# Kernel optimization log

Measured on AMD Instinct MI355X. Metric: run time of the kernel, lower is better.

Reference implementation:

```python
import jax, jax.numpy as jnp
import numpy as np

N_NODES = 16384
N_EDGES = 131072
N_GRAPHS = 16
U_SZ, U_RED = 4096, 256
EDGE_H, EDGE_OUT = 1024, 512
NODE_H = 512
NODE_IN = 9  # 4 + 5, hard-coded in OGRENet
EDGE_IN = 1


def _lin_init(k, fan_in, fan_out):
    k1, k2 = jax.random.split(k)
    bound = 1.0 / np.sqrt(fan_in)
    W = jax.random.uniform(k1, (fan_in, fan_out), jnp.float32, -bound, bound)
    b = jax.random.uniform(k2, (fan_out,), jnp.float32, -bound, bound)
    return W, b


def setup_inputs() -> dict:
    key = jax.random.key(0)
    ks = jax.random.split(key, 16)
    inp = {
        "x": jax.random.normal(ks[0], (N_NODES, NODE_IN), jnp.float32),
        "edge_attr": jax.random.normal(ks[1], (N_EDGES, EDGE_IN), jnp.float32),
        "u": jax.random.normal(ks[2], (N_GRAPHS, U_SZ), jnp.float32),
        "edge_index": jax.random.randint(ks[3], (2, N_EDGES), 0, N_NODES, jnp.int64 if jax.config.jax_enable_x64 else jnp.int32).astype(jnp.int32),
        "batch": jnp.sort(jax.random.randint(ks[4], (N_NODES,), 0, N_GRAPHS)).astype(jnp.int32),
    }
    # global dim reduction 4096 -> 256
    inp["w_dr"], inp["b_dr"] = _lin_init(ks[5], U_SZ, U_RED)
    # edge MLP: in = 1 + 2*9 + 256 = 275
    e_in = EDGE_IN + 2 * NODE_IN + U_RED
    inp["e_w0"], inp["e_b0"] = _lin_init(ks[6], e_in, EDGE_H)
    inp["e_w1"], inp["e_b1"] = _lin_init(ks[7], EDGE_H, EDGE_H)
    inp["e_w2"], inp["e_b2"] = _lin_init(ks[8], EDGE_H, EDGE_H)
    inp["e_w3"], inp["e_b3"] = _lin_init(ks[9], EDGE_H, EDGE_H)
    inp["e_wf"], inp["e_bf"] = _lin_init(ks[10], EDGE_H, EDGE_OUT)
    # node mlp 1: in = 9 + 512 = 521
    inp["n1_w0"], inp["n1_b0"] = _lin_init(ks[11], NODE_IN + EDGE_OUT, NODE_H)
    inp["n1_w1"], inp["n1_b1"] = _lin_init(ks[12], NODE_H, NODE_H)
    # node mlp 2: in = 9 + 512 + 256 = 777, out = 1
    inp["n2_w0"], inp["n2_b0"] = _lin_init(ks[13], NODE_IN + NODE_H + U_RED, NODE_H)
    inp["n2_w1"], inp["n2_b1"] = _lin_init(ks[14], NODE_H, 1)
    return inp


def reference(x, edge_attr, u, edge_index, batch,
              w_dr, b_dr,
              e_w0, e_b0, e_w1, e_b1, e_w2, e_b2, e_w3, e_b3, e_wf, e_bf,
              n1_w0, n1_b0, n1_w1, n1_b1,
              n2_w0, n2_b0, n2_w1, n2_b1):
    relu = jax.nn.relu
    # select_dim_reduction
    u_r = u @ w_dr + b_dr  # [G, 256]
    row, col = edge_index[0], edge_index[1]
    # EdgeModel: cat([src, dest, edge_attr, u[batch[row]]])
    e_in = jnp.concatenate([x[row], x[col], edge_attr, u_r[batch[row]]], axis=1)
    h = relu(e_in @ e_w0 + e_b0)
    h = relu(h @ e_w1 + e_b1)
    h = relu(h @ e_w2 + e_b2)
    h = relu(h @ e_w3 + e_b3)
    e = h @ e_wf + e_bf  # [E, 512]
    # NodeModel: mlp1 on cat([x[col], edge_attr_new]) then scatter_mean by row
    n_in = jnp.concatenate([x[col], e], axis=1)
    h = relu(n_in @ n1_w0 + n1_b0)
    h = relu(h @ n1_w1 + n1_b1)  # [E, 512]
    agg = jax.ops.segment_sum(h, row, num_segments=N_NODES)
    cnt = jax.ops.segment_sum(jnp.ones((h.shape[0],), h.dtype), row, num_segments=N_NODES)
    agg = agg / jnp.maximum(cnt, 1.0)[:, None]  # scatter_mean (zeros stay zero)
    o = jnp.concatenate([x, agg, u_r[batch]], axis=1)
    o = relu(o @ n2_w0 + n2_b0) @ n2_w1 + n2_b1  # [N, 1]
    return jnp.squeeze(o, axis=-1)
```

## Files before the change

### kernel.cpp

```cpp
#include <hip/hip_runtime.h>
#include <type_traits>
#include <utility>
#include <cstdint>

typedef unsigned short u16;
typedef __attribute__((ext_vector_type(4))) float f32x4;
typedef __attribute__((ext_vector_type(8))) short s16x8;
typedef __attribute__((ext_vector_type(8))) __bf16 b16x8;

template <typename T, typename = void> struct MfmaTakes : std::false_type {};
template <typename T>
struct MfmaTakes<T, std::void_t<decltype(__builtin_amdgcn_mfma_f32_16x16x32_bf16(
    std::declval<T>(), std::declval<T>(), std::declval<f32x4>(), 0, 0, 0))>>
    : std::true_type {};
using abvec = std::conditional_t<MfmaTakes<s16x8>::value, s16x8, b16x8>;
static_assert(sizeof(abvec) == 16, "frag must be 4 VGPRs");

template <typename T>
__device__ __forceinline__ f32x4 mfma_bf16(T a, T b, f32x4 c) {
  return __builtin_amdgcn_mfma_f32_16x16x32_bf16(a, b, c, 0, 0, 0);
}

__device__ __forceinline__ float b2f(u16 v) {
  union { unsigned u; float f; } x; x.u = ((unsigned)v) << 16; return x.f;
}
__device__ __forceinline__ u16 f2b(float f) {
  union { float f; unsigned u; } x; x.f = f;
  unsigned r = x.u + 0x7fffu + ((x.u >> 16) & 1u);
  return (u16)(r >> 16);
}

__device__ __forceinline__ void gld16(const void* g, void* l) {
  auto gp = reinterpret_cast<const __attribute__((address_space(1))) unsigned int*>(
      reinterpret_cast<uintptr_t>(g));
  auto lp = reinterpret_cast<__attribute__((address_space(3))) unsigned int*>(
      reinterpret_cast<uintptr_t>(l));
  __builtin_amdgcn_global_load_lds(gp, lp, 16, 0, 0);
}

#define NN 16384
#define NE 131072
#define NG 16

__global__ void detect_dtype(const u16* __restrict__ x, int* __restrict__ flag) {
  __shared__ int cnt;
  if (threadIdx.x == 0) cnt = 0;
  __syncthreads();
  int local = 0;
#pragma unroll
  for (int i = 0; i < 8; i++) {
    u16 h = x[threadIdx.x * 8 + i];
    int e = (h >> 7) & 0xFF;
    if (h == 0 || (e >= 110 && e <= 134)) local++;
  }
  atomicAdd(&cnt, local);
  __syncthreads();
  if (threadIdx.x == 0) *flag = (cnt >= 1700) ? 1 : 0;
}

struct CvtJob {
  const void* src[14];
  void* dst[14];
  int n[14];
};

__global__ __launch_bounds__(256) void cvt_all(CvtJob jb, const int* __restrict__ flag) {
  const int idx = blockIdx.x * 256 + threadIdx.x;
  const int f = *flag;
  int off = 0;
#pragma unroll
  for (int j = 0; j < 14; j++) {
    const int nn = jb.n[j];
    if (idx < off + nn) {
      const int i = idx - off;
      u16 v = f ? ((const u16*)jb.src[j])[i]
                : f2b(((const float*)jb.src[j])[i]);
      ((u16*)jb.dst[j])[i] = v;
      return;
    }
    off += nn;
  }
}

__global__ __launch_bounds__(256) void cvt_plain(
    const void* __restrict__ src, u16* __restrict__ dst, int n,
    const int* __restrict__ flag)
{
  const int i = blockIdx.x * 256 + threadIdx.x;
  if (i >= n) return;
  dst[i] = *flag ? ((const u16*)src)[i] : f2b(((const float*)src)[i]);
}

__global__ __launch_bounds__(256, 3) void gemm_bt(
    const u16* __restrict__ A, const u16* __restrict__ Bt,
    const u16* __restrict__ bias, u16* __restrict__ C,
    int M, int N, int K, int ldc, int relu)
{
  __shared__ alignas(16) u16 smem[24576];
  const int tid = threadIdx.x;
  const int wave = tid >> 6, lane = tid & 63;
  const int m0 = blockIdx.x * 128, n0 = blockIdx.y * 128;

  const int srow = lane >> 2;
  const int kslot = lane & 3;
  const int sswz = (srow >> 1) & 3;
  const u16* gA = A + (size_t)(m0 + wave * 32 + srow) * K + (kslot ^ sswz) * 8;
  const u16* gB = Bt + (size_t)(n0 + wave * 32 + srow) * K + (kslot ^ sswz) * 8;
  const int loff = (wave * 32 + srow) * 32 + kslot * 8;

  const int wm = (wave >> 1) * 64;
  const int wn = (wave & 1) * 64;
  const int fr = lane & 15;
  const int fks = ((lane >> 4) ^ ((fr >> 1) & 3)) * 8;

  f32x4 acc[4][4] = {};
  const int NT = K >> 5;

#define STAGE(t, s) do { \
    const int o_ = (t) * 32; \
    u16* S_ = smem + (s) * 8192; \
    gld16(gA + o_, S_ + loff); gld16(gA + 16 * (size_t)K + o_, S_ + loff + 512); \
    gld16(gB + o_, S_ + 4096 + loff); gld16(gB + 16 * (size_t)K + o_, S_ + 4096 + loff + 512); \
  } while (0)

  STAGE(0, 0);
  if (NT > 1) {
    STAGE(1, 1);
    __asm__ volatile("s_waitcnt vmcnt(4)" ::: "memory");
  } else {
    __asm__ volatile("s_waitcnt vmcnt(0)" ::: "memory");
  }
  __builtin_amdgcn_s_barrier();

  int sl = 0;
  for (int t = 0; t < NT; t++) {
    if (t + 2 < NT) {
      const int sw = (sl + 2 >= 3) ? sl - 1 : sl + 2;
      STAGE(t + 2, sw);
    }
    const u16* As = smem + sl * 8192;
    const u16* Bs = As + 4096;
    abvec af[4], bf[4];
#pragma unroll
    for (int i = 0; i < 4; i++)
      af[i] = *(const abvec*)&As[(wm + i * 16 + fr) * 32 + fks];
#pragma unroll
    for (int i = 0; i < 4; i++)
      bf[i] = *(const abvec*)&Bs[(wn + i * 16 + fr) * 32 + fks];
    __builtin_amdgcn_s_setprio(1);
#pragma unroll
    for (int mi = 0; mi < 4; mi++)
#pragma unroll
      for (int ni = 0; ni < 4; ni++)
        acc[mi][ni] = mfma_bf16(af[mi], bf[ni], acc[mi][ni]);
    __builtin_amdgcn_s_setprio(0);
    if (t + 2 < NT) __asm__ volatile("s_waitcnt vmcnt(4)" ::: "memory");
    else            __asm__ volatile("s_waitcnt vmcnt(0)" ::: "memory");
    __builtin_amdgcn_s_barrier();
    sl = (sl == 2) ? 0 : sl + 1;
  }
#undef STAGE

  const int crow0 = (lane >> 4) * 4;
  float bv[4];
#pragma unroll
  for (int ni = 0; ni < 4; ni++) bv[ni] = b2f(bias[n0 + wn + ni * 16 + fr]);

  u16* W = smem + wave * 4096;
#pragma unroll
  for (int mi = 0; mi < 4; mi++) {
#pragma unroll
    for (int ni = 0; ni < 4; ni++) {
      f32x4 v = acc[mi][ni];
      const int colx = ni * 16 + fr;
      const int cl = colx & 7, ch = colx >> 3;
#pragma unroll
      for (int r = 0; r < 4; r++) {
        const int rowx = mi * 16 + crow0 + r;
        float f = v[r] + bv[ni];
        if (relu) f = fmaxf(f, 0.0f);
        W[rowx * 64 + ((ch ^ (rowx & 7)) << 3) + cl] = f2b(f);
      }
    }
  }
  __asm__ volatile("s_waitcnt lgkmcnt(0)" ::: "memory");
#pragma unroll
  for (int p = 0; p < 8; p++) {
    const int rowx = p * 8 + (lane >> 3);
    const int pc = lane & 7;
    const int lc = pc ^ (rowx & 7);
    s16x8 val = *(const s16x8*)&W[rowx * 64 + pc * 8];
    *(s16x8*)&C[(size_t)(m0 + wm + rowx) * ldc + n0 + wn + lc * 8] = val;
  }
}

__global__ __launch_bounds__(256, 3) void gemm_bt_rb(
    const u16* __restrict__ A, const u16* __restrict__ Bt,
    const u16* __restrict__ bias, u16* __restrict__ C,
    int M, int N, int K, int ldc, int relu,
    const u16* __restrict__ rb, const int* __restrict__ ridx, int rbs)
{
  __shared__ alignas(16) u16 smem[24576];
  const int tid = threadIdx.x;
  const int wave = tid >> 6, lane = tid & 63;
  const int m0 = blockIdx.x * 128, n0 = blockIdx.y * 128;

  const int srow = lane >> 2;
  const int kslot = lane & 3;
  const int sswz = (srow >> 1) & 3;
  const u16* gA = A + (size_t)(m0 + wave * 32 + srow) * K + (kslot ^ sswz) * 8;
  const u16* gB = Bt + (size_t)(n0 + wave * 32 + srow) * K + (kslot ^ sswz) * 8;
  const int loff = (wave * 32 + srow) * 32 + kslot * 8;

  const int wm = (wave >> 1) * 64;
  const int wn = (wave & 1) * 64;
  const int fr = lane & 15;
  const int fks = ((lane >> 4) ^ ((fr >> 1) & 3)) * 8;

  f32x4 acc[4][4] = {};
  const int NT = K >> 5;

#define STAGE(t, s) do { \
    const int o_ = (t) * 32; \
    u16* S_ = smem + (s) * 8192; \
    gld16(gA + o_, S_ + loff); gld16(gA + 16 * (size_t)K + o_, S_ + loff + 512); \
    gld16(gB + o_, S_ + 4096 + loff); gld16(gB + 16 * (size_t)K + o_, S_ + 4096 + loff + 512); \
  } while (0)

  STAGE(0, 0);
  if (NT > 1) {
    STAGE(1, 1);
    __asm__ volatile("s_waitcnt vmcnt(4)" ::: "memory");
  } else {
    __asm__ volatile("s_waitcnt vmcnt(0)" ::: "memory");
  }
  __builtin_amdgcn_s_barrier();

  int sl = 0;
  for (int t = 0; t < NT; t++) {
    if (t + 2 < NT) {
      const int sw = (sl + 2 >= 3) ? sl - 1 : sl + 2;
      STAGE(t + 2, sw);
    }
    const u16* As = smem + sl * 8192;
    const u16* Bs = As + 4096;
    abvec af[4], bf[4];
#pragma unroll
    for (int i = 0; i < 4; i++)
      af[i] = *(const abvec*)&As[(wm + i * 16 + fr) * 32 + fks];
#pragma unroll
    for (int i = 0; i < 4; i++)
      bf[i] = *(const abvec*)&Bs[(wn + i * 16 + fr) * 32 + fks];
    __builtin_amdgcn_s_setprio(1);
#pragma unroll
    for (int mi = 0; mi < 4; mi++)
#pragma unroll
      for (int ni = 0; ni < 4; ni++)
        acc[mi][ni] = mfma_bf16(af[mi], bf[ni], acc[mi][ni]);
    __builtin_amdgcn_s_setprio(0);
    if (t + 2 < NT) __asm__ volatile("s_waitcnt vmcnt(4)" ::: "memory");
    else            __asm__ volatile("s_waitcnt vmcnt(0)" ::: "memory");
    __builtin_amdgcn_s_barrier();
    sl = (sl == 2) ? 0 : sl + 1;
  }
#undef STAGE

  const int crow0 = (lane >> 4) * 4;
  float bv[4];
#pragma unroll
  for (int ni = 0; ni < 4; ni++) bv[ni] = b2f(bias[n0 + wn + ni * 16 + fr]);

  u16* W = smem + wave * 4096;
#pragma unroll
  for (int mi = 0; mi < 4; mi++) {
#pragma unroll
    for (int ni = 0; ni < 4; ni++) {
      f32x4 v = acc[mi][ni];
      const int colx = ni * 16 + fr;
      const int cl = colx & 7, ch = colx >> 3;
#pragma unroll
      for (int r = 0; r < 4; r++) {
        const int rowx = mi * 16 + crow0 + r;
        float f = v[r] + bv[ni]
                + b2f(rb[(size_t)ridx[m0 + wm + rowx] * rbs + n0 + wn + ni * 16 + fr]);
        if (relu) f = fmaxf(f, 0.0f);
        W[rowx * 64 + ((ch ^ (rowx & 7)) << 3) + cl] = f2b(f);
      }
    }
  }
  __asm__ volatile("s_waitcnt lgkmcnt(0)" ::: "memory");
#pragma unroll
  for (int p = 0; p < 8; p++) {
    const int rowx = p * 8 + (lane >> 3);
    const int pc = lane & 7;
    const int lc = pc ^ (rowx & 7);
    s16x8 val = *(const s16x8*)&W[rowx * 64 + pc * 8];
    *(s16x8*)&C[(size_t)(m0 + wm + rowx) * ldc + n0 + wn + lc * 8] = val;
  }
}

__global__ __launch_bounds__(1024) void gemm256b(
    const u16* __restrict__ A, const u16* __restrict__ Bt,
    const u16* __restrict__ bias, u16* __restrict__ C,
    int K, int ldc, int relu)
{
  __shared__ alignas(16) u16 smem[49152];
  const int tid = threadIdx.x;
  const int wave = tid >> 6, lane = tid & 63;
  const int wr = wave >> 2, wc = wave & 3;
  const int m0 = blockIdx.x << 8, n0 = blockIdx.y << 8;

  const int srow = tid >> 2;
  const int kslot = tid & 3;
  const int sswz = (srow >> 1) & 3;
  const u16* gA = A  + (size_t)(m0 + srow) * K + (kslot ^ sswz) * 8;
  const u16* gB = Bt + (size_t)(n0 + srow) * K + (kslot ^ sswz) * 8;
  const int loff = tid * 8;

  const int fr = lane & 15;
  const int fks = ((lane >> 4) ^ ((fr >> 1) & 3)) * 8;
  const int aob = (wr * 64 + fr) * 32 + fks;
  const int bob = (wc * 64 + fr) * 32 + fks;

  f32x4 acc[4][4] = {};
  const int NT = K >> 5;

#define STAGE2(t, s) do { \
    const int o_ = (t) * 32; \
    u16* S_ = smem + (s) * 16384; \
    gld16(gA + o_, S_ + loff); gld16(gB + o_, S_ + 8192 + loff); \
  } while (0)

  STAGE2(0, 0);
  if (NT > 1) {
    STAGE2(1, 1);
    __asm__ volatile("s_waitcnt vmcnt(2)" ::: "memory");
  } else {
    __asm__ volatile("s_waitcnt vmcnt(0)" ::: "memory");
  }
  __builtin_amdgcn_s_barrier();

  int sl = 0;
  for (int t = 0; t < NT; t++) {
    if (t + 2 < NT) {
      const int sw = (sl + 2 >= 3) ? sl - 1 : sl + 2;
      STAGE2(t + 2, sw);
    }
    const u16* As = smem + sl * 16384;
    const u16* Bs = As + 8192;
    abvec af[4], bf[4];
#pragma unroll
    for (int i = 0; i < 4; i++)
      af[i] = *(const abvec*)&As[aob + i * 512];
#pragma unroll
    for (int i = 0; i < 4; i++)
      bf[i] = *(const abvec*)&Bs[bob + i * 512];
    __builtin_amdgcn_s_setprio(1);
#pragma unroll
    for (int mi = 0; mi < 4; mi++)
#pragma unroll
      for (int ni = 0; ni < 4; ni++)
        acc[mi][ni] = mfma_bf16(af[mi], bf[ni], acc[mi][ni]);
    __builtin_amdgcn_s_setprio(0);
    if (t + 2 < NT) __asm__ volatile("s_waitcnt vmcnt(2)" ::: "memory");
    else            __asm__ volatile("s_waitcnt vmcnt(0)" ::: "memory");
    __builtin_amdgcn_s_barrier();
    sl = (sl == 2) ? 0 : sl + 1;
  }
#undef STAGE2

  const int crow0 = (lane >> 4) * 4;
  float bv[4];
#pragma unroll
  for (int ni = 0; ni < 4; ni++) bv[ni] = b2f(bias[n0 + wc * 64 + ni * 16 + fr]);
  u16* W = smem + wave * 2048;
#pragma unroll
  for (int h = 0; h < 2; h++) {
    if (h) __asm__ volatile("s_waitcnt lgkmcnt(0)" ::: "memory");
#pragma unroll
    for (int mi = 0; mi < 4; mi++) {
#pragma unroll
      for (int nh = 0; nh < 2; nh++) {
        const int ni = h * 2 + nh;
        f32x4 v = acc[mi][ni];
        const int colx = nh * 16 + fr;
        const int cl = colx & 7, ch = colx >> 3;
#pragma unroll
        for (int r = 0; r < 4; r++) {
          const int rowx = mi * 16 + crow0 + r;
          float f = v[r] + bv[ni];
          if (relu) f = fmaxf(f, 0.0f);
          W[rowx * 32 + ((ch ^ (rowx & 3)) << 3) + cl] = f2b(f);
        }
      }
    }
    __asm__ volatile("s_waitcnt lgkmcnt(0)" ::: "memory");
#pragma unroll
    for (int p = 0; p < 4; p++) {
      const int rowx = p * 16 + (lane >> 2);
      const int pc = lane & 3;
      const int lc = pc ^ (rowx & 3);
      s16x8 val = *(const s16x8*)&W[rowx * 32 + pc * 8];
      *(s16x8*)&C[(size_t)(m0 + wr * 64 + rowx) * ldc + n0 + wc * 64 + h * 32 + lc * 8] = val;
    }
  }
}

__global__ __launch_bounds__(1024) void gemm256b_rb(
    const u16* __restrict__ A, const u16* __restrict__ Bt,
    const u16* __restrict__ bias, u16* __restrict__ C,
    int K, int ldc, int relu,
    const u16* __restrict__ rb, const int* __restrict__ ridx, int rbs)
{
  __shared__ alignas(16) u16 smem[49152];
  const int tid = threadIdx.x;
  const int wave = tid >> 6, lane = tid & 63;
  const int wr = wave >> 2, wc = wave & 3;
  const int m0 = blockIdx.x << 8, n0 = blockIdx.y << 8;

  const int srow = tid >> 2;
  const int kslot = tid & 3;
  const int sswz = (srow >> 1) & 3;
  const u16* gA = A  + (size_t)(m0 + srow) * K + (kslot ^ sswz) * 8;
  const u16* gB = Bt + (size_t)(n0 + srow) * K + (kslot ^ sswz) * 8;
  const int loff = tid * 8;

  const int fr = lane & 15;
  const int fks = ((lane >> 4) ^ ((fr >> 1) & 3)) * 8;
  const int aob = (wr * 64 + fr) * 32 + fks;
  const int bob = (wc * 64 + fr) * 32 + fks;

  f32x4 acc[4][4] = {};
  const int NT = K >> 5;

#define STAGE2(t, s) do { \
    const int o_ = (t) * 32; \
    u16* S_ = smem + (s) * 16384; \
    gld16(gA + o_, S_ + loff); gld16(gB + o_, S_ + 8192 + loff); \
  } while (0)

  STAGE2(0, 0);
  if (NT > 1) {
    STAGE2(1, 1);
    __asm__ volatile("s_waitcnt vmcnt(2)" ::: "memory");
  } else {
    __asm__ volatile("s_waitcnt vmcnt(0)" ::: "memory");
  }
  __builtin_amdgcn_s_barrier();

  int sl = 0;
  for (int t = 0; t < NT; t++) {
    if (t + 2 < NT) {
      const int sw = (sl + 2 >= 3) ? sl - 1 : sl + 2;
      STAGE2(t + 2, sw);
    }
    const u16* As = smem + sl * 16384;
    const u16* Bs = As + 8192;
    abvec af[4], bf[4];
#pragma unroll
    for (int i = 0; i < 4; i++)
      af[i] = *(const abvec*)&As[aob + i * 512];
#pragma unroll
    for (int i = 0; i < 4; i++)
      bf[i] = *(const abvec*)&Bs[bob + i * 512];
    __builtin_amdgcn_s_setprio(1);
#pragma unroll
    for (int mi = 0; mi < 4; mi++)
#pragma unroll
      for (int ni = 0; ni < 4; ni++)
        acc[mi][ni] = mfma_bf16(af[mi], bf[ni], acc[mi][ni]);
    __builtin_amdgcn_s_setprio(0);
    if (t + 2 < NT) __asm__ volatile("s_waitcnt vmcnt(2)" ::: "memory");
    else            __asm__ volatile("s_waitcnt vmcnt(0)" ::: "memory");
    __builtin_amdgcn_s_barrier();
    sl = (sl == 2) ? 0 : sl + 1;
  }
#undef STAGE2

  const int crow0 = (lane >> 4) * 4;
  float bv[4];
#pragma unroll
  for (int ni = 0; ni < 4; ni++) bv[ni] = b2f(bias[n0 + wc * 64 + ni * 16 + fr]);
  u16* W = smem + wave * 2048;
#pragma unroll
  for (int h = 0; h < 2; h++) {
    if (h) __asm__ volatile("s_waitcnt lgkmcnt(0)" ::: "memory");
#pragma unroll
    for (int mi = 0; mi < 4; mi++) {
#pragma unroll
      for (int nh = 0; nh < 2; nh++) {
        const int ni = h * 2 + nh;
        f32x4 v = acc[mi][ni];
        const int colx = nh * 16 + fr;
        const int cl = colx & 7, ch = colx >> 3;
#pragma unroll
        for (int r = 0; r < 4; r++) {
          const int rowx = mi * 16 + crow0 + r;
          float f = v[r] + bv[ni]
                  + b2f(rb[(size_t)ridx[m0 + wr * 64 + rowx] * rbs + n0 + wc * 64 + ni * 16 + fr]);
          if (relu) f = fmaxf(f, 0.0f);
          W[rowx * 32 + ((ch ^ (rowx & 3)) << 3) + cl] = f2b(f);
        }
      }
    }
    __asm__ volatile("s_waitcnt lgkmcnt(0)" ::: "memory");
#pragma unroll
    for (int p = 0; p < 4; p++) {
      const int rowx = p * 16 + (lane >> 2);
      const int pc = lane & 3;
      const int lc = pc ^ (rowx & 3);
      s16x8 val = *(const s16x8*)&W[rowx * 32 + pc * 8];
      *(s16x8*)&C[(size_t)(m0 + wr * 64 + rowx) * ldc + n0 + wc * 64 + h * 32 + lc * 8] = val;
    }
  }
}

__global__ __launch_bounds__(256) void transpose_pad(
    const void* __restrict__ src, u16* __restrict__ dst, int K, int N, int Kp,
    int perm, int k0, const int* __restrict__ flag)
{
  __shared__ u16 tile[32][33];
  const int f = *flag;
  const u16* s16p = (const u16*)src;
  const float* sfp = (const float*)src;
  const int kb = blockIdx.x * 32, nb = blockIdx.y * 32;
  const int tx = threadIdx.x & 31, ty = threadIdx.x >> 5;
#pragma unroll
  for (int i = 0; i < 32; i += 8) {
    int k = kb + ty + i, n = nb + tx;
    u16 v = 0;
    if (k < K && n < N)
      v = f ? s16p[(size_t)(k0 + k) * N + n] : f2b(sfp[(size_t)(k0 + k) * N + n]);
    tile[ty + i][tx] = v;
  }
  __syncthreads();
#pragma unroll
  for (int i = 0; i < 32; i += 8) {
    int n = nb + ty + i, k = kb + tx;
    if (n < N && k < Kp) {
      int nk = perm ? (k < 9 ? 512 + k : (k < 521 ? k - 9 : k)) : k;
      dst[(size_t)n * Kp + nk] = tile[tx][ty + i];
    }
  }
}

__global__ __launch_bounds__(256) void fuse_tail(
    const u16* __restrict__ n1w0t, u16* __restrict__ fused)
{
  const int idx = blockIdx.x * 256 + threadIdx.x;
  const int p = idx >> 5, t = idx & 31;
  fused[p * 1056 + 1024 + t] = n1w0t[p * 544 + 512 + t];
}

__global__ __launch_bounds__(256) void fuse_bias(
    const u16* __restrict__ ebf, const u16* __restrict__ n1b0,
    const u16* __restrict__ n1w0e, u16* __restrict__ fb)
{
  const int p = blockIdx.x * 256 + threadIdx.x;
  float acc = b2f(n1b0[p]);
#pragma unroll 8
  for (int j = 0; j < 512; j++) acc += b2f(ebf[j]) * b2f(n1w0e[p * 512 + j]);
  fb[p] = f2b(acc);
}

__global__ __launch_bounds__(256) void make_uwb(
    const void* __restrict__ w0, const u16* __restrict__ ur,
    const u16* __restrict__ eb0, u16* __restrict__ uwb,
    const int* __restrict__ flag)
{
  const int g = blockIdx.x;
  const int n = blockIdx.y * 256 + threadIdx.x;
  const int f = *flag;
  __shared__ u16 us[256];
  us[threadIdx.x] = ur[g * 256 + threadIdx.x];
  __syncthreads();
  float acc = b2f(eb0[n]);
  if (f) {
    const u16* wp = (const u16*)w0 + 19ull * 1024 + n;
#pragma unroll 8
    for (int j = 0; j < 256; j++) acc += b2f(us[j]) * b2f(wp[(size_t)j * 1024]);
  } else {
    const float* wp = (const float*)w0 + 19ull * 1024 + n;
#pragma unroll 8
    for (int j = 0; j < 256; j++) acc += b2f(us[j]) * wp[(size_t)j * 1024];
  }
  uwb[g * 1024 + n] = f2b(acc);
}

__global__ __launch_bounds__(256) void make_uw2(
    const void* __restrict__ w, const u16* __restrict__ ur,
    const u16* __restrict__ b0, u16* __restrict__ uw2,
    const int* __restrict__ flag)
{
  const int g = blockIdx.x;
  const int p = blockIdx.y * 256 + threadIdx.x;
  const int f = *flag;
  __shared__ u16 us[256];
  us[threadIdx.x] = ur[g * 256 + threadIdx.x];
  __syncthreads();
  float acc = b2f(b0[p]);
  if (f) {
    const u16* wp = (const u16*)w + 521ull * 512 + p;
#pragma unroll 8
    for (int j = 0; j < 256; j++) acc += b2f(us[j]) * b2f(wp[(size_t)j * 512]);
  } else {
    const float* wp = (const float*)w + 521ull * 512 + p;
#pragma unroll 8
    for (int j = 0; j < 256; j++) acc += b2f(us[j]) * wp[(size_t)j * 512];
  }
  uw2[g * 512 + p] = f2b(acc);
}

__global__ __launch_bounds__(256) void dim_reduce2(
    const u16* __restrict__ u, const void* __restrict__ w,
    float* __restrict__ uacc, const int* __restrict__ flag)
{
  const int g = blockIdx.x, kt = blockIdx.y, j = threadIdx.x;
  const int f = *flag;
  __shared__ u16 us[512];
  us[j] = u[g * 4096 + kt * 512 + j];
  us[256 + j] = u[g * 4096 + kt * 512 + 256 + j];
  __syncthreads();
  float acc = 0.0f;
  if (f) {
    const u16* wp = (const u16*)w + (size_t)(kt * 512) * 256 + j;
#pragma unroll 8
    for (int k = 0; k < 512; k++) acc += b2f(us[k]) * b2f(wp[(size_t)k * 256]);
  } else {
    const float* wp = (const float*)w + (size_t)(kt * 512) * 256 + j;
#pragma unroll 8
    for (int k = 0; k < 512; k++) acc += b2f(us[k]) * wp[(size_t)k * 256];
  }
  atomicAdd(&uacc[g * 256 + j], acc);
}

__global__ __launch_bounds__(256) void finish_ur(
    const float* __restrict__ uacc, const u16* __restrict__ bdr,
    u16* __restrict__ ur)
{
  const int i = blockIdx.x * 256 + threadIdx.x;
  ur[i] = f2b(uacc[i] + b2f(bdr[i & 255]));
}

__global__ __launch_bounds__(256) void count_edges(
    const int* __restrict__ row, int* __restrict__ cnt)
{
  const int e = blockIdx.x * 256 + threadIdx.x;
  if (e < NE) atomicAdd(&cnt[row[e]], 1);
}

__global__ __launch_bounds__(256) void prefix_offs(
    const int* __restrict__ cnt, int* __restrict__ offs, int* __restrict__ cursor)
{
  __shared__ int part[256];
  __shared__ int base[256];
  const int t = threadIdx.x;
  int s = 0;
#pragma unroll
  for (int i = 0; i < 64; i++) s += cnt[t * 64 + i];
  part[t] = s;
  __syncthreads();
  if (t == 0) {
    int r = 0;
    for (int i = 0; i < 256; i++) { base[i] = r; r += part[i]; }
  }
  __syncthreads();
  int r = base[t];
#pragma unroll
  for (int i = 0; i < 64; i++) {
    const int n = t * 64 + i;
    offs[n] = r; cursor[n] = r; r += cnt[n];
  }
  if (t == 255) offs[16384] = r;
}

__global__ __launch_bounds__(256) void build_perm(
    const int* __restrict__ row, int* __restrict__ cursor, int* __restrict__ eperm)
{
  const int e = blockIdx.x * 256 + threadIdx.x;
  const int pos = atomicAdd(&cursor[row[e]], 1);
  eperm[pos] = e;
}

__global__ __launch_bounds__(256) void build_ein2(
    const u16* __restrict__ x, const u16* __restrict__ ea,
    const int* __restrict__ row, const int* __restrict__ col,
    const int* __restrict__ batch, const int* __restrict__ eperm,
    u16* __restrict__ out, int* __restrict__ bidx, int e0)
{
  const int idx = blockIdx.x * 256 + threadIdx.x;
  const int le = idx >> 2, g = idx & 3;
  const int c0 = g * 8;
  const int e = eperm[e0 + le];
  const int r = row[e];
  const int cl = col[e];
  if (g == 0) bidx[le] = batch[r];
  alignas(16) u16 v[8];
#pragma unroll
  for (int j = 0; j < 8; j++) {
    const int c = c0 + j;
    u16 t;
    if (c < 9)        t = x[r * 9 + c];
    else if (c < 18)  t = x[cl * 9 + (c - 9)];
    else if (c == 18) t = ea[e];
    else              t = 0;
    v[j] = t;
  }
  *(s16x8*)&out[(size_t)le * 32 + c0] = *(const s16x8*)v;
}

__global__ __launch_bounds__(256) void fill_h_tail(
    const u16* __restrict__ x, const int* __restrict__ col,
    const int* __restrict__ eperm, u16* __restrict__ out, int e0)
{
  const int idx = blockIdx.x * 256 + threadIdx.x;
  const int le = idx >> 2, j8 = idx & 3;
  const int c0 = 1024 + j8 * 8;
  const int cl = col[eperm[e0 + le]];
  alignas(16) u16 v[8];
#pragma unroll
  for (int j = 0; j < 8; j++) {
    const int c = c0 + j;
    v[j] = (c < 1033) ? x[cl * 9 + (c - 1024)] : (u16)0;
  }
  *(s16x8*)&out[(size_t)le * 1056 + c0] = *(const s16x8*)v;
}

__global__ __launch_bounds__(256) void seg_reduce(
    const u16* __restrict__ h, const int* __restrict__ offs,
    float* __restrict__ agg, int e0, int echunk)
{
  const int wave = threadIdx.x >> 6, lane = threadIdx.x & 63;
  const int n = blockIdx.x * 4 + wave;
  int lo = offs[n], hi = offs[n + 1];
  const int first = (lo >= e0);
  lo = lo > e0 ? lo : e0;
  const int e1 = e0 + echunk;
  hi = hi < e1 ? hi : e1;
  if (lo >= hi) return;
  const int c0 = lane * 8;
  float acc[8] = {};
  for (int i = lo; i < hi; i++) {
    s16x8 v = *(const s16x8*)&h[(size_t)(i - e0) * 512 + c0];
#pragma unroll
    for (int j = 0; j < 8; j++) acc[j] += b2f((u16)v[j]);
  }
  float* ap = &agg[(size_t)n * 512 + c0];
  if (first) {
#pragma unroll
    for (int j = 0; j < 8; j++) ap[j] = acc[j];
  } else {
#pragma unroll
    for (int j = 0; j < 8; j++) ap[j] += acc[j];
  }
}

__global__ __launch_bounds__(256) void build_nin2(
    const u16* __restrict__ x, const float* __restrict__ agg,
    const int* __restrict__ cnt, u16* __restrict__ out, int n0)
{
  const int idx = blockIdx.x * 256 + threadIdx.x;
  const int le = idx / 68, g = idx % 68;
  const int c0 = g * 8;
  const int n = n0 + le;
  alignas(16) u16 v[8];
  if (c0 < 512) {
    const int cn = cnt[n];
    if (cn == 0) {
#pragma unroll
      for (int j = 0; j < 8; j++) v[j] = 0;
    } else {
      const float den = (float)cn;
      const f32x4* ap = (const f32x4*)&agg[(size_t)n * 512 + c0];
      f32x4 a0 = ap[0], a1 = ap[1];
#pragma unroll
      for (int j = 0; j < 4; j++) { v[j] = f2b(a0[j] / den); v[4 + j] = f2b(a1[j] / den); }
    }
  } else {
#pragma unroll
    for (int j = 0; j < 8; j++) {
      const int c = c0 + j;
      v[j] = (c < 521) ? x[n * 9 + (c - 512)] : (u16)0;
    }
  }
  *(s16x8*)&out[(size_t)le * 544 + c0] = *(const s16x8*)v;
}

__global__ __launch_bounds__(256) void final_dot(
    const u16* __restrict__ h, const u16* __restrict__ w,
    const u16* __restrict__ b, void* __restrict__ out, int n0,
    const int* __restrict__ flag)
{
  const int wave = threadIdx.x >> 6, lane = threadIdx.x & 63;
  const int n = blockIdx.x * 4 + wave;
  const u16* hp = h + (size_t)n * 512 + lane * 8;
  const u16* wp = w + lane * 8;
  float s = 0.0f;
#pragma unroll
  for (int i = 0; i < 8; i++) s += b2f(hp[i]) * b2f(wp[i]);
#pragma unroll
  for (int off = 32; off > 0; off >>= 1) s += __shfl_down(s, off, 64);
  if (lane == 0) {
    float r = s + b2f(b[0]);
    if (*flag) ((u16*)out)[n0 + n] = f2b(r);
    else       ((float*)out)[n0 + n] = r;
  }
}

constexpr size_t OFF_FLAG = 0;
constexpr size_t OFF_XC   = 64;
constexpr size_t OFF_EAC  = OFF_XC   + 147456ull * 2;
constexpr size_t OFF_UC   = OFF_EAC  + 131072ull * 2;
constexpr size_t OFF_BDR  = OFF_UC   + 65536ull * 2;
constexpr size_t OFF_EB0  = OFF_BDR  + 256ull * 2;
constexpr size_t OFF_EB1  = OFF_EB0  + 1024ull * 2;
constexpr size_t OFF_EB2  = OFF_EB1  + 1024ull * 2;
constexpr size_t OFF_EB3  = OFF_EB2  + 1024ull * 2;
constexpr size_t OFF_EBF  = OFF_EB3  + 1024ull * 2;
constexpr size_t OFF_N1B0 = OFF_EBF  + 512ull * 2;
constexpr size_t OFF_N1B1 = OFF_N1B0 + 512ull * 2;
constexpr size_t OFF_N2B0 = OFF_N1B1 + 512ull * 2;
constexpr size_t OFF_N2W1 = OFF_N2B0 + 512ull * 2;
constexpr size_t OFF_N2B1 = OFF_N2W1 + 512ull * 2;
constexpr size_t OFF_OFFS = (OFF_N2B1 + 64 + 63) & ~63ull;
constexpr size_t OFF_CUR  = OFF_OFFS + 16388ull * 4;
constexpr size_t OFF_UACC = OFF_CUR  + 16384ull * 4;
static_assert(OFF_UACC + 4096 * 4 < (1ull << 20), "params+small fit in 1MB");

constexpr size_t OFF_W0T  = 1ull << 20;
constexpr size_t OFF_W1T  = OFF_W0T  + 1024ull * 320 * 2;
constexpr size_t OFF_W2T  = OFF_W1T  + 1024ull * 1024 * 2;
constexpr size_t OFF_W3T  = OFF_W2T  + 1024ull * 1024 * 2;
constexpr size_t OFF_WFC  = OFF_W3T  + 1024ull * 1024 * 2;
constexpr size_t OFF_N1W0 = OFF_WFC  + 1024ull * 512 * 2;
constexpr size_t OFF_N1W1 = OFF_N1W0 + 512ull * 544 * 2;
constexpr size_t OFF_N2W0 = OFF_N1W1 + 512ull * 512 * 2;
constexpr size_t OFF_N1WE = OFF_N2W0 + 512ull * 800 * 2;
constexpr size_t OFF_FUSE = OFF_N1WE + 512ull * 512 * 2;
constexpr size_t OFF_FB   = OFF_FUSE + 512ull * 1056 * 2;
constexpr size_t OFF_ZB   = OFF_FB   + 512ull * 2;
constexpr size_t OFF_UWB  = OFF_ZB   + 1024ull * 2;
constexpr size_t OFF_UW2  = OFF_UWB  + 16384ull * 2;
constexpr size_t OFF_UR   = OFF_UW2  + 8192ull * 2;
constexpr size_t OFF_CNT  = OFF_UR   + 16ull * 256 * 2;
constexpr size_t OFF_AGG  = OFF_CNT  + 16384ull * 4;
constexpr size_t OFF_BUF0 = OFF_AGG  + 16384ull * 512 * 4;

extern "C" void kernel_launch(void* const* d_in, const int* in_sizes, int n_in,
                              void* d_out, int out_size, void* d_ws, size_t ws_size,
                              hipStream_t stream) {
  const void* x_r  = d_in[0];
  const void* ea_r = d_in[1];
  const void* u_r  = d_in[2];
  const int*  ei    = (const int*)d_in[3];
  const int*  batch = (const int*)d_in[4];
  const void* w_dr = d_in[5];
  const void* b_dr = d_in[6];
  const void* e_w0 = d_in[7];  const void* e_b0 = d_in[8];
  const void* e_w1 = d_in[9];  const void* e_b1 = d_in[10];
  const void* e_w2 = d_in[11]; const void* e_b2 = d_in[12];
  const void* e_w3 = d_in[13]; const void* e_b3 = d_in[14];
  const void* e_wf = d_in[15]; const void* e_bf = d_in[16];
  const void* n1w0 = d_in[17]; const void* n1b0 = d_in[18];
  const void* n1w1 = d_in[19]; const void* n1b1 = d_in[20];
  const void* n2w0 = d_in[21]; const void* n2b0 = d_in[22];
  const void* n2w1 = d_in[23]; const void* n2b1 = d_in[24];

  const int* row = ei;
  const int* col = ei + NE;

  char* ws = (char*)d_ws;
  int*   FLAG = (int*)(ws + OFF_FLAG);
  u16*   XC   = (u16*)(ws + OFF_XC);
  u16*   EAC  = (u16*)(ws + OFF_EAC);
  u16*   UC   = (u16*)(ws + OFF_UC);
  u16*   BDRC = (u16*)(ws + OFF_BDR);
  u16*   EB0C = (u16*)(ws + OFF_EB0);
  u16*   EB1C = (u16*)(ws + OFF_EB1);
  u16*   EB2C = (u16*)(ws + OFF_EB2);
  u16*   EB3C = (u16*)(ws + OFF_EB3);
  u16*   EBFC = (u16*)(ws + OFF_EBF);
  u16*   N1B0C= (u16*)(ws + OFF_N1B0);
  u16*   N1B1C= (u16*)(ws + OFF_N1B1);
  u16*   N2B0C= (u16*)(ws + OFF_N2B0);
  u16*   N2W1C= (u16*)(ws + OFF_N2W1);
  u16*   N2B1C= (u16*)(ws + OFF_N2B1);
  int*   OFFS = (int*)(ws + OFF_OFFS);
  int*   CUR  = (int*)(ws + OFF_CUR);
  float* UACC = (float*)(ws + OFF_UACC);
  u16*   W0T  = (u16*)(ws + OFF_W0T);
  u16*   W1T  = (u16*)(ws + OFF_W1T);
  u16*   W2T  = (u16*)(ws + OFF_W2T);
  u16*   W3T  = (u16*)(ws + OFF_W3T);
  u16*   WFC  = (u16*)(ws + OFF_WFC);
  u16*   N1W0T= (u16*)(ws + OFF_N1W0);
  u16*   N1W1T= (u16*)(ws + OFF_N1W1);
  u16*   N2W0T= (u16*)(ws + OFF_N2W0);
  u16*   N1WE = (u16*)(ws + OFF_N1WE);
  u16*   FUSED= (u16*)(ws + OFF_FUSE);
  u16*   FB   = (u16*)(ws + OFF_FB);
  u16*   ZB   = (u16*)(ws + OFF_ZB);
  u16*   UWB  = (u16*)(ws + OFF_UWB);
  u16*   UW2  = (u16*)(ws + OFF_UW2);
  u16*   UR   = (u16*)(ws + OFF_UR);
  int*   CNT  = (int*)(ws + OFF_CNT);
  float* AGG  = (float*)(ws + OFF_AGG);
  (void)in_sizes; (void)n_in; (void)out_size;

  int echunk = 16384;
  while (echunk > 2048 &&
         OFF_BUF0 + (size_t)echunk * 4228 + (size_t)NE * 4 > ws_size) echunk >>= 1;
  u16* P    = (u16*)(ws + OFF_BUF0);
  u16* Q    = (u16*)(ws + OFF_BUF0 + (size_t)echunk * 2112);
  int* EPRM = (int*)(ws + OFF_BUF0 + (size_t)echunk * 4224);
  int* BIDX = EPRM + NE;
  const int nchunks = NE / echunk;
  const int nodch = echunk < NN ? echunk : NN;
  const int nodchn = NN / nodch;

  detect_dtype<<<1, 256, 0, stream>>>((const u16*)x_r, FLAG);

  CvtJob jb;
  const void* srcs[14] = {x_r, ea_r, u_r, b_dr, e_b0, e_b1, e_b2, e_b3,
                          e_bf, n1b0, n1b1, n2b0, n2w1, n2b1};
  void* dsts[14] = {XC, EAC, UC, BDRC, EB0C, EB1C, EB2C, EB3C,
                    EBFC, N1B0C, N1B1C, N2B0C, N2W1C, N2B1C};
  const int ns[14] = {147456, 131072, 65536, 256, 1024, 1024, 1024, 1024,
                      512, 512, 512, 512, 512, 1};
  int tot = 0;
  for (int j = 0; j < 14; j++) { jb.src[j] = srcs[j]; jb.dst[j] = dsts[j]; jb.n[j] = ns[j]; tot += ns[j]; }
  cvt_all<<<(tot + 255) / 256, 256, 0, stream>>>(jb, FLAG);

  transpose_pad<<<dim3(1, 32),  256, 0, stream>>>(e_w0, W0T,   19, 1024, 32, 0, 0, FLAG);
  transpose_pad<<<dim3(32, 32), 256, 0, stream>>>(e_w1, W1T, 1024, 1024, 1024, 0, 0, FLAG);
  transpose_pad<<<dim3(32, 32), 256, 0, stream>>>(e_w2, W2T, 1024, 1024, 1024, 0, 0, FLAG);
  transpose_pad<<<dim3(32, 32), 256, 0, stream>>>(e_w3, W3T, 1024, 1024, 1024, 0, 0, FLAG);
  transpose_pad<<<dim3(17, 16), 256, 0, stream>>>(n1w0, N1W0T, 521, 512, 544, 1, 0, FLAG);
  transpose_pad<<<dim3(16, 16), 256, 0, stream>>>(n1w1, N1W1T, 512, 512, 512, 0, 0, FLAG);
  transpose_pad<<<dim3(17, 16), 256, 0, stream>>>(n2w0, N2W0T, 521, 512, 544, 1, 0, FLAG);
  transpose_pad<<<dim3(16, 16), 256, 0, stream>>>(n1w0, N1WE, 512, 512, 512, 0, 9, FLAG);
  cvt_plain<<<2048, 256, 0, stream>>>(e_wf, WFC, 1024 * 512, FLAG);

  (void)hipMemsetAsync(UACC, 0, 4096ull * 4, stream);
  (void)hipMemsetAsync(CNT, 0, 16384ull * 4, stream);
  (void)hipMemsetAsync(ZB, 0, 2048, stream);

  gemm_bt<<<dim3(4, 8), 256, 0, stream>>>(N1WE, WFC, ZB, FUSED, 512, 1024, 512, 1056, 0);
  fuse_tail<<<64, 256, 0, stream>>>(N1W0T, FUSED);
  fuse_bias<<<2, 256, 0, stream>>>(EBFC, N1B0C, N1WE, FB);

  dim_reduce2<<<dim3(NG, 8), 256, 0, stream>>>(UC, w_dr, UACC, FLAG);
  finish_ur<<<16, 256, 0, stream>>>(UACC, BDRC, UR);
  make_uwb<<<dim3(16, 4), 256, 0, stream>>>(e_w0, UR, EB0C, UWB, FLAG);
  make_uw2<<<dim3(16, 2), 256, 0, stream>>>(n2w0, UR, N2B0C, UW2, FLAG);

  count_edges<<<NE / 256, 256, 0, stream>>>(row, CNT);
  prefix_offs<<<1, 256, 0, stream>>>(CNT, OFFS, CUR);
  build_perm<<<NE / 256, 256, 0, stream>>>(row, CUR, EPRM);

  for (int c = 0; c < nchunks; c++) {
    const int e0 = c * echunk;
    build_ein2<<<echunk * 4 / 256, 256, 0, stream>>>(XC, EAC, row, col, batch, EPRM, P, BIDX, e0);
    gemm256b_rb<<<dim3(echunk / 256, 4), 1024, 0, stream>>>(P, W0T, ZB, Q, 32, 1024, 1,
                                                            UWB, BIDX, 1024);
    gemm256b<<<dim3(echunk / 256, 4), 1024, 0, stream>>>(Q, W1T, EB1C, P, 1024, 1024, 1);
    gemm256b<<<dim3(echunk / 256, 4), 1024, 0, stream>>>(P, W2T, EB2C, Q, 1024, 1024, 1);
    gemm256b<<<dim3(echunk / 256, 4), 1024, 0, stream>>>(Q, W3T, EB3C, P, 1024, 1056, 1);
    fill_h_tail<<<echunk * 4 / 256, 256, 0, stream>>>(XC, col, EPRM, P, e0);
    gemm_bt<<<dim3(echunk / 128, 4), 256, 0, stream>>>(P, FUSED, FB, Q, echunk, 512, 1056, 512, 1);
    gemm_bt<<<dim3(echunk / 128, 4), 256, 0, stream>>>(Q, N1W1T, N1B1C, P, echunk, 512, 512, 512, 1);
    seg_reduce<<<NN / 4, 256, 0, stream>>>(P, OFFS, AGG, e0, echunk);
  }

  for (int c = 0; c < nodchn; c++) {
    const int n0 = c * nodch;
    build_nin2<<<nodch * 68 / 256, 256, 0, stream>>>(XC, AGG, CNT, P, n0);
    gemm_bt_rb<<<dim3(nodch / 128, 4), 256, 0, stream>>>(P, N2W0T, ZB, Q, nodch, 512, 544, 512, 1,
                                                         UW2, batch + n0, 512);
    final_dot<<<nodch / 4, 256, 0, stream>>>(Q, N2W1C, N2B1C, d_out, n0, FLAG);
  }
}
```

Before: 1.673 ms.

## Add 4-stage pipelined 256-tile GEMM, larger edge chunks, big-tile node MLP

After: 1.472 ms. 1.14x faster.

```diff
diff --git a/kernel.cpp b/kernel.cpp
--- a/kernel.cpp
+++ b/kernel.cpp
@@ -366,6 +366,114 @@
     else            __asm__ volatile("s_waitcnt vmcnt(0)" ::: "memory");
     __builtin_amdgcn_s_barrier();
     sl = (sl == 2) ? 0 : sl + 1;
+  }
+#undef STAGE2
+
+  const int crow0 = (lane >> 4) * 4;
+  float bv[4];
+#pragma unroll
+  for (int ni = 0; ni < 4; ni++) bv[ni] = b2f(bias[n0 + wc * 64 + ni * 16 + fr]);
+  u16* W = smem + wave * 2048;
+#pragma unroll
+  for (int h = 0; h < 2; h++) {
+    if (h) __asm__ volatile("s_waitcnt lgkmcnt(0)" ::: "memory");
+#pragma unroll
+    for (int mi = 0; mi < 4; mi++) {
+#pragma unroll
+      for (int nh = 0; nh < 2; nh++) {
+        const int ni = h * 2 + nh;
+        f32x4 v = acc[mi][ni];
+        const int colx = nh * 16 + fr;
+        const int cl = colx & 7, ch = colx >> 3;
+#pragma unroll
+        for (int r = 0; r < 4; r++) {
+          const int rowx = mi * 16 + crow0 + r;
+          float f = v[r] + bv[ni];
+          if (relu) f = fmaxf(f, 0.0f);
+          W[rowx * 32 + ((ch ^ (rowx & 3)) << 3) + cl] = f2b(f);
+        }
+      }
+    }
+    __asm__ volatile("s_waitcnt lgkmcnt(0)" ::: "memory");
+#pragma unroll
+    for (int p = 0; p < 4; p++) {
+      const int rowx = p * 16 + (lane >> 2);
+      const int pc = lane & 3;
+      const int lc = pc ^ (rowx & 3);
+      s16x8 val = *(const s16x8*)&W[rowx * 32 + pc * 8];
+      *(s16x8*)&C[(size_t)(m0 + wr * 64 + rowx) * ldc + n0 + wc * 64 + h * 32 + lc * 8] = val;
+    }
+  }
+}
+
+__global__ __launch_bounds__(1024) void gemm256c(
+    const u16* __restrict__ A, const u16* __restrict__ Bt,
+    const u16* __restrict__ bias, u16* __restrict__ C,
+    int K, int ldc, int relu)
+{
+  __shared__ alignas(16) u16 smem[65536];
+  const int tid = threadIdx.x;
+  const int wave = tid >> 6, lane = tid & 63;
+  const int wr = wave >> 2, wc = wave & 3;
+  const int m0 = blockIdx.x << 8, n0 = blockIdx.y << 8;
+
+  const int srow = tid >> 2;
+  const int kslot = tid & 3;
+  const int sswz = (srow >> 1) & 3;
+  const u16* gA = A  + (size_t)(m0 + srow) * K + (kslot ^ sswz) * 8;
+  const u16* gB = Bt + (size_t)(n0 + srow) * K + (kslot ^ sswz) * 8;
+  const int loff = tid * 8;
+
+  const int fr = lane & 15;
+  const int fks = ((lane >> 4) ^ ((fr >> 1) & 3)) * 8;
+  const int aob = (wr * 64 + fr) * 32 + fks;
+  const int bob = (wc * 64 + fr) * 32 + fks;
+
+  f32x4 acc[4][4] = {};
+  const int NT = K >> 5;
+
+#define STAGE2(t, s) do { \
+    const int o_ = (t) * 32; \
+    u16* S_ = smem + (s) * 16384; \
+    gld16(gA + o_, S_ + loff); gld16(gB + o_, S_ + 8192 + loff); \
+  } while (0)
+
+  STAGE2(0, 0);
+  if (NT > 2) {
+    STAGE2(1, 1); STAGE2(2, 2);
+    __asm__ volatile("s_waitcnt vmcnt(4)" ::: "memory");
+  } else if (NT > 1) {
+    STAGE2(1, 1);
+    __asm__ volatile("s_waitcnt vmcnt(2)" ::: "memory");
+  } else {
+    __asm__ volatile("s_waitcnt vmcnt(0)" ::: "memory");
+  }
+  __builtin_amdgcn_s_barrier();
+
+  int sl = 0;
+  for (int t = 0; t < NT; t++) {
+    if (t + 3 < NT) STAGE2(t + 3, (sl + 3) & 3);
+    const u16* As = smem + sl * 16384;
+    const u16* Bs = As + 8192;
+    abvec af[4], bf[4];
+#pragma unroll
+    for (int i = 0; i < 4; i++)
+      af[i] = *(const abvec*)&As[aob + i * 512];
+#pragma unroll
+    for (int i = 0; i < 4; i++)
+      bf[i] = *(const abvec*)&Bs[bob + i * 512];
+    __builtin_amdgcn_s_setprio(1);
+#pragma unroll
+    for (int mi = 0; mi < 4; mi++)
+#pragma unroll
+      for (int ni = 0; ni < 4; ni++)
+        acc[mi][ni] = mfma_bf16(af[mi], bf[ni], acc[mi][ni]);
+    __builtin_amdgcn_s_setprio(0);
+    if (t + 3 < NT)      __asm__ volatile("s_waitcnt vmcnt(4)" ::: "memory");
+    else if (t + 2 < NT) __asm__ volatile("s_waitcnt vmcnt(2)" ::: "memory");
+    else                 __asm__ volatile("s_waitcnt vmcnt(0)" ::: "memory");
+    __builtin_amdgcn_s_barrier();
+    sl = (sl + 1) & 3;
   }
 #undef STAGE2
 
@@ -907,7 +1015,7 @@
   float* AGG  = (float*)(ws + OFF_AGG);
   (void)in_sizes; (void)n_in; (void)out_size;
 
-  int echunk = 16384;
+  int echunk = 32768;
   while (echunk > 2048 &&
          OFF_BUF0 + (size_t)echunk * 4228 + (size_t)NE * 4 > ws_size) echunk >>= 1;
   u16* P    = (u16*)(ws + OFF_BUF0);
@@ -963,12 +1071,23 @@
     build_ein2<<<echunk * 4 / 256, 256, 0, stream>>>(XC, EAC, row, col, batch, EPRM, P, BIDX, e0);
     gemm256b_rb<<<dim3(echunk / 256, 4), 1024, 0, stream>>>(P, W0T, ZB, Q, 32, 1024, 1,
                                                             UWB, BIDX, 1024);
-    gemm256b<<<dim3(echunk / 256, 4), 1024, 0, stream>>>(Q, W1T, EB1C, P, 1024, 1024, 1);
-    gemm256b<<<dim3(echunk / 256, 4), 1024, 0, stream>>>(P, W2T, EB2C, Q, 1024, 1024, 1);
-    gemm256b<<<dim3(echunk / 256, 4), 1024, 0, stream>>>(Q, W3T, EB3C, P, 1024, 1056, 1);
+    if (c & 1) {
+      gemm256b<<<dim3(echunk / 256, 4), 1024, 0, stream>>>(Q, W1T, EB1C, P, 1024, 1024, 1);
+      gemm256b<<<dim3(echunk / 256, 4), 1024, 0, stream>>>(P, W2T, EB2C, Q, 1024, 1024, 1);
+      gemm256b<<<dim3(echunk / 256, 4), 1024, 0, stream>>>(Q, W3T, EB3C, P, 1024, 1056, 1);
+    } else {
+      gemm256c<<<dim3(echunk / 256, 4), 1024, 0, stream>>>(Q, W1T, EB1C, P, 1024, 1024, 1);
+      gemm256c<<<dim3(echunk / 256, 4), 1024, 0, stream>>>(P, W2T, EB2C, Q, 1024, 1024, 1);
+      gemm256c<<<dim3(echunk / 256, 4), 1024, 0, stream>>>(Q, W3T, EB3C, P, 1024, 1056, 1);
+    }
     fill_h_tail<<<echunk * 4 / 256, 256, 0, stream>>>(XC, col, EPRM, P, e0);
-    gemm_bt<<<dim3(echunk / 128, 4), 256, 0, stream>>>(P, FUSED, FB, Q, echunk, 512, 1056, 512, 1);
-    gemm_bt<<<dim3(echunk / 128, 4), 256, 0, stream>>>(Q, N1W1T, N1B1C, P, echunk, 512, 512, 512, 1);
+    if (echunk >= 32768) {
+      gemm256b<<<dim3(echunk / 256, 2), 1024, 0, stream>>>(P, FUSED, FB, Q, 1056, 512, 1);
+      gemm256b<<<dim3(echunk / 256, 2), 1024, 0, stream>>>(Q, N1W1T, N1B1C, P, 512, 512, 1);
+    } else {
+      gemm_bt<<<dim3(echunk / 128, 4), 256, 0, stream>>>(P, FUSED, FB, Q, echunk, 512, 1056, 512, 1);
+      gemm_bt<<<dim3(echunk / 128, 4), 256, 0, stream>>>(Q, N1W1T, N1B1C, P, echunk, 512, 512, 512, 1);
+    }
     seg_reduce<<<NN / 4, 256, 0, stream>>>(P, OFFS, AGG, e0, echunk);
   }
 
```
